# Optimization experiments

Measured on AMD Instinct MI355X. Metric: run time of the kernel, lower is better.

The kernel has to match this reference:

```python
import jax, jax.numpy as jnp
import numpy as np

LATENT = 1024

def setup_inputs() -> dict:
    key = jax.random.key(0)
    ks = jax.random.split(key, 8)
    N, BD, H, W = 1024, 2048, 7, 7
    C = 64  # num classes (pos == orient, required by stack dim=2)
    feat = jax.random.normal(ks[0], (N, BD, H, W), dtype=jnp.float32)
    fc1_w = jax.random.normal(ks[1], (LATENT, BD), dtype=jnp.float32) * (2.0 / BD) ** 0.5
    fc1_b = jnp.zeros((LATENT,), dtype=jnp.float32)
    cls_pos_w = jax.random.normal(ks[2], (C, LATENT), dtype=jnp.float32) * (2.0 / LATENT) ** 0.5
    cls_pos_b = jnp.zeros((C,), dtype=jnp.float32)
    cls_orient_w = jax.random.normal(ks[3], (C, LATENT), dtype=jnp.float32) * (2.0 / LATENT) ** 0.5
    cls_orient_b = jnp.zeros((C,), dtype=jnp.float32)
    reg_pos_w = jax.random.normal(ks[4], (C, 3, LATENT), dtype=jnp.float32) * (2.0 / LATENT) ** 0.5
    reg_pos_b = jnp.zeros((C, 3), dtype=jnp.float32)
    reg_orient_w = jax.random.normal(ks[5], (C, 4, LATENT), dtype=jnp.float32) * (2.0 / LATENT) ** 0.5
    reg_orient_b = jnp.zeros((C, 4), dtype=jnp.float32)
    return {"feat": feat, "fc1_w": fc1_w, "fc1_b": fc1_b,
            "cls_pos_w": cls_pos_w, "cls_pos_b": cls_pos_b,
            "cls_orient_w": cls_orient_w, "cls_orient_b": cls_orient_b,
            "reg_pos_w": reg_pos_w, "reg_pos_b": reg_pos_b,
            "reg_orient_w": reg_orient_w, "reg_orient_b": reg_orient_b}

def _to_label(pred):
    # relu(sum(cumprod(pred > 0.5, dim=1)) - 1) -> int64 ordinal label
    run = jnp.cumprod((pred > 0.5).astype(jnp.int32), axis=1)
    return jnp.maximum(run.sum(axis=1) - 1, 0).astype(jnp.int32)

def reference(feat, fc1_w, fc1_b, cls_pos_w, cls_pos_b, cls_orient_w, cls_orient_b,
              reg_pos_w, reg_pos_b, reg_orient_w, reg_orient_b):
    # AdaptiveAvgPool2d(1) + flatten -> [N, backbone_dim]
    x = feat.mean(axis=(2, 3))
    # fc1 + ReLU (dropout is identity at inference)
    x = jax.nn.relu(x @ fc1_w.T + fc1_b)  # [N, latent]
    cls_x = jax.nn.sigmoid(x @ cls_pos_w.T + cls_pos_b)      # [N, C]
    cls_q = jax.nn.sigmoid(x @ cls_orient_w.T + cls_orient_b)  # [N, C]
    idx_x = _to_label(cls_x)
    idx_q = _to_label(cls_q)
    # Hard-routed expert heads: gather per-sample expert weights, batched matvec
    p_x = jnp.einsum('nkd,nd->nk', reg_pos_w[idx_x], x) + reg_pos_b[idx_x]        # [N, 3]
    p_q = jnp.einsum('nkd,nd->nk', reg_orient_w[idx_q], x) + reg_orient_b[idx_q]  # [N, 4]
    pose = jnp.concatenate([p_x, p_q], axis=1)       # [N, 7]
    pose_cls = jnp.stack([cls_x, cls_q], axis=2)     # [N, C, 2]
    return pose, pose_cls
```

## Files before the change

kernel.cpp:

```cpp
#include <hip/hip_runtime.h>
#include <hip/hip_bf16.h>

#define N_SAMP   1024
#define BD       2048
#define LATENT_D 1024
#define NCLS     64
#define HW       49

typedef __attribute__((ext_vector_type(8))) _Float16 f16x8;
typedef __attribute__((ext_vector_type(4))) float f32x4;
typedef unsigned short u16;

__device__ __forceinline__ size_t split_idx_r(int row, int k, int rows) {
    const int kg = k >> 5, ke = k & 31;
    const int c2 = (ke * 2) ^ (((row >> 1) & 3) << 4);
    return ((size_t)(kg * rows + row) * 32) + (c2 >> 1);
}

__device__ __forceinline__ void split2(float v, u16* p0, u16* p1, size_t idx) {
    _Float16 h0 = (_Float16)v;
    _Float16 h1 = (_Float16)(v - (float)h0);
    p0[idx] = *(u16*)&h0;
    p1[idx] = *(u16*)&h1;
}

#define GLL16(g, l) __builtin_amdgcn_global_load_lds( \
    (const __attribute__((address_space(1))) void*)(g), \
    (__attribute__((address_space(3))) void*)(l), 16, 0, 0)

__global__ __launch_bounds__(256) void prep_kernel(const float* __restrict__ feat,
                                                   const float* __restrict__ W,
                                                   const float* __restrict__ Wp,
                                                   const float* __restrict__ Wo,
                                                   u16* __restrict__ a0,
                                                   u16* __restrict__ a1,
                                                   u16* __restrict__ b0,
                                                   u16* __restrict__ b1,
                                                   u16* __restrict__ c0,
                                                   u16* __restrict__ c1) {
    __shared__ float buf[256 * HW];
    const int b = blockIdx.x;
    const int tid = threadIdx.x;
    if (b < 8192) {
        const int lane = tid & 63, wv = tid >> 6;
        const float* src = feat + (size_t)b * (256 * HW);
        for (int c = wv; c < 49; c += 4)
            GLL16(src + c * 256 + lane * 4, (char*)buf + c * 1024 + lane * 16);
        asm volatile("s_waitcnt vmcnt(0)" ::: "memory");
        __syncthreads();
        const float* p = buf + tid * HW;
        float s = 0.f;
        #pragma unroll
        for (int k = 0; k < HW; ++k) s += p[k];
        const float v = s * (1.0f / 49.0f);
        const int n = b >> 3;
        const int d = (b & 7) * 256 + tid;
        split2(v, a0, a1, split_idx_r(n, d, N_SAMP));
    } else if (b < 16384) {
        const int b2 = b - 8192;
        const int row = b2 >> 3;
        const int d = (b2 & 7) * 256 + tid;
        split2(W[(size_t)row * BD + d], b0, b1, split_idx_r(row, d, LATENT_D));
    } else {
        const int b2 = b - 16384;
        const int row = b2 >> 2;
        const int d = (b2 & 3) * 256 + tid;
        const float v = row < 64 ? Wp[(size_t)row * LATENT_D + d]
                                 : Wo[(size_t)(row - 64) * LATENT_D + d];
        split2(v, c0, c1, split_idx_r(row, d, 128));
    }
}

__global__ __launch_bounds__(256, 2) void split_mfma(
    const u16* __restrict__ A0, const u16* __restrict__ A1,
    const u16* __restrict__ B0, const u16* __restrict__ B1,
    float* __restrict__ part, int ksteps, int rowsA, int rowsB, int ldc) {
    __shared__ u16 lds[2][4 * 4096];
    const int nwg = gridDim.x * gridDim.y * gridDim.z;
    const int flat = blockIdx.x + gridDim.x * (blockIdx.y + gridDim.y * blockIdx.z);
    const int chunk = nwg >> 3;
    const int swz = (flat & 7) * chunk + (flat >> 3);
    const int bn = swz % gridDim.x;
    const int rest = swz / gridDim.x;
    const int bm = rest % gridDim.y;
    const int kz = rest / gridDim.y;

    const int tid = threadIdx.x, lane = tid & 63, wv = tid >> 6;
    const int wrow = (wv >> 1) * 64, wcol = (wv & 1) * 64;
    const int r15 = lane & 15, khi = lane >> 4;

    const u16* gA[2] = {A0, A1};
    const u16* gB[2] = {B0, B1};
    const int kg0 = kz * ksteps;

    auto stage = [&](int kg, int buf) {
        #pragma unroll
        for (int s = 0; s < 2; ++s) {
            const u16* g = gA[s] + ((size_t)(kg * rowsA + bm * 128 + wv * 32) * 32) + lane * 8;
            u16* l = &lds[buf][s * 4096 + wv * 1024 + lane * 8];
            GLL16(g, l);
            GLL16(g + 512, l + 512);
        }
        #pragma unroll
        for (int s = 0; s < 2; ++s) {
            const u16* g = gB[s] + ((size_t)(kg * rowsB + bn * 128 + wv * 32) * 32) + lane * 8;
            u16* l = &lds[buf][(2 + s) * 4096 + wv * 1024 + lane * 8];
            GLL16(g, l);
            GLL16(g + 512, l + 512);
        }
    };

    f32x4 acc[4][4];
    #pragma unroll
    for (int i = 0; i < 4; ++i)
        #pragma unroll
        for (int j = 0; j < 4; ++j) acc[i][j] = (f32x4){0.f, 0.f, 0.f, 0.f};

    stage(kg0, 0);
    asm volatile("s_waitcnt vmcnt(0)" ::: "memory");
    __builtin_amdgcn_s_barrier();

    int cur = 0;
    for (int ks = 0; ks < ksteps; ++ks) {
        f16x8 af[4][2], bf[4][2];
        #pragma unroll
        for (int i = 0; i < 4; ++i) {
            const int rowA = wrow + i * 16 + r15;
            const int offA = rowA * 64 + ((khi * 16) ^ (((rowA >> 1) & 3) << 4));
            const int rowB = wcol + i * 16 + r15;
            const int offB = rowB * 64 + ((khi * 16) ^ (((rowB >> 1) & 3) << 4));
            #pragma unroll
            for (int s = 0; s < 2; ++s) {
                af[i][s] = *(const f16x8*)((const char*)&lds[cur][s * 4096] + offA);
                bf[i][s] = *(const f16x8*)((const char*)&lds[cur][(2 + s) * 4096] + offB);
            }
        }
        if (ks + 1 < ksteps) stage(kg0 + ks + 1, cur ^ 1);
        #pragma unroll
        for (int p = 0; p < 3; ++p) {
            const int pa = (p == 2) ? 1 : 0;
            const int pb = (p == 1) ? 1 : 0;
            #pragma unroll
            for (int i = 0; i < 4; ++i)
                #pragma unroll
                for (int j = 0; j < 4; ++j)
                    acc[i][j] = __builtin_amdgcn_mfma_f32_16x16x32_f16(
                        af[i][pa], bf[j][pb], acc[i][j], 0, 0, 0);
        }
        asm volatile("s_waitcnt vmcnt(0)" ::: "memory");
        __builtin_amdgcn_s_barrier();
        cur ^= 1;
    }

    float* pt = part + (size_t)kz * ((size_t)N_SAMP * ldc);
    #pragma unroll
    for (int i = 0; i < 4; ++i) {
        const int row0 = bm * 128 + wrow + i * 16 + khi * 4;
        #pragma unroll
        for (int j = 0; j < 4; ++j) {
            const int col = bn * 128 + wcol + j * 16 + r15;
            #pragma unroll
            for (int q = 0; q < 4; ++q)
                pt[(size_t)(row0 + q) * ldc + col] = acc[i][j][q];
        }
    }
}

__global__ __launch_bounds__(256) void reduce_fc1(const float* __restrict__ part,
                                                  const float* __restrict__ bias,
                                                  float* __restrict__ x,
                                                  u16* __restrict__ x0,
                                                  u16* __restrict__ x1,
                                                  int nsplit) {
    const int i = blockIdx.x * 256 + threadIdx.x;
    const float4* p = reinterpret_cast<const float4*>(part);
    float4 s = p[i];
    for (int z = 1; z < nsplit; ++z) {
        const float4 t = p[(size_t)z * 262144 + i];
        s.x += t.x; s.y += t.y; s.z += t.z; s.w += t.w;
    }
    const float4 b = reinterpret_cast<const float4*>(bias)[i & 255];
    s.x = fmaxf(s.x + b.x, 0.f); s.y = fmaxf(s.y + b.y, 0.f);
    s.z = fmaxf(s.z + b.z, 0.f); s.w = fmaxf(s.w + b.w, 0.f);
    reinterpret_cast<float4*>(x)[i] = s;
    const int n = i >> 8, d0 = (i & 255) * 4;
    split2(s.x, x0, x1, split_idx_r(n, d0 + 0, N_SAMP));
    split2(s.y, x0, x1, split_idx_r(n, d0 + 1, N_SAMP));
    split2(s.z, x0, x1, split_idx_r(n, d0 + 2, N_SAMP));
    split2(s.w, x0, x1, split_idx_r(n, d0 + 3, N_SAMP));
}

__global__ __launch_bounds__(128) void decode_expert(const float* __restrict__ part2,
                                                     const float* __restrict__ bp,
                                                     const float* __restrict__ bo,
                                                     const float* __restrict__ x,
                                                     const float* __restrict__ wpos,
                                                     const float* __restrict__ bpos,
                                                     const float* __restrict__ wori,
                                                     const float* __restrict__ bori,
                                                     float* __restrict__ pose_cls,
                                                     float* __restrict__ pose,
                                                     int nsplit) {
    const int n = blockIdx.x, t = threadIdx.x;
    __shared__ float xs[LATENT_D];
    __shared__ int esh[2];

    const float4* x4 = reinterpret_cast<const float4*>(x + (size_t)n * LATENT_D);
    float4* xs4 = reinterpret_cast<float4*>(xs);
    xs4[t] = x4[t];
    xs4[t + 128] = x4[t + 128];

    float s = (t < 64) ? bp[t] : bo[t - 64];
    for (int z = 0; z < nsplit; ++z)
        s += part2[(size_t)z * (N_SAMP * 128) + (size_t)n * 128 + t];
    const float sig = 1.0f / (1.0f + expf(-s));
    const int head = t >> 6, c = t & 63;
    pose_cls[(size_t)n * (NCLS * 2) + c * 2 + head] = sig;

    const unsigned long long mask = __ballot(s > 0.0f);
    if (c == 0) {
        const unsigned long long inv = ~mask;
        const int run = inv ? __builtin_ctzll(inv) : 64;
        const int lab = run - 1;
        esh[head] = lab > 0 ? lab : 0;
    }
    __syncthreads();

    const int e = esh[head];
    const int nk = head ? 4 : 3;
    for (int kk = 0; kk < nk; ++kk) {
        const float* wr = head ? wori + (size_t)(e * 4 + kk) * LATENT_D
                               : wpos + (size_t)(e * 3 + kk) * LATENT_D;
        const float bb = head ? bori[e * 4 + kk] : bpos[e * 3 + kk];
        const float4* w4 = reinterpret_cast<const float4*>(wr);
        float s2 = 0.f;
        #pragma unroll
        for (int i = 0; i < 4; ++i) {
            const int q = c + i * 64;
            const float4 a = w4[q];
            s2 += a.x * xs[q * 4] + a.y * xs[q * 4 + 1] + a.z * xs[q * 4 + 2] + a.w * xs[q * 4 + 3];
        }
        #pragma unroll
        for (int off = 32; off > 0; off >>= 1) s2 += __shfl_down(s2, off);
        if (c == 0) pose[(size_t)n * 7 + (head ? 3 + kk : kk)] = s2 + bb;
    }
}

extern "C" void kernel_launch(void* const* d_in, const int* in_sizes, int n_in,
                              void* d_out, int out_size, void* d_ws, size_t ws_size,
                              hipStream_t stream) {
    const float* feat   = (const float*)d_in[0];
    const float* fc1_w  = (const float*)d_in[1];
    const float* fc1_b  = (const float*)d_in[2];
    const float* cpw    = (const float*)d_in[3];
    const float* cpb    = (const float*)d_in[4];
    const float* cow    = (const float*)d_in[5];
    const float* cob    = (const float*)d_in[6];
    const float* rpw    = (const float*)d_in[7];
    const float* rpb    = (const float*)d_in[8];
    const float* row_   = (const float*)d_in[9];
    const float* rob    = (const float*)d_in[10];

    float* out = (float*)d_out;
    float* pose     = out;
    float* pose_cls = out + (size_t)N_SAMP * 7;

    char* ws = (char*)d_ws;
    const size_t MB = (size_t)1 << 20;
    size_t off = 0;
    auto take = [&](size_t bytes) { char* p = ws + off; off += (bytes + 255) & ~(size_t)255; return p; };

    u16* A0 = (u16*)take(4 * MB);
    u16* A1 = (u16*)take(4 * MB);
    u16* B0 = (u16*)take(4 * MB);
    u16* B1 = (u16*)take(4 * MB);
    u16* C0 = (u16*)take(256 * 1024);
    u16* C1 = (u16*)take(256 * 1024);
    u16* X0 = (u16*)take(2 * MB);
    u16* X1 = (u16*)take(2 * MB);
    float* x = (float*)take(4 * MB);

    int nsplit = 8;
    while (nsplit > 1 && off + (size_t)nsplit * 4 * MB + 3 * MB > ws_size) nsplit >>= 1;
    float* part = (float*)take((size_t)nsplit * 4 * MB);
    int nsplit_c = 4;
    while (nsplit_c > 1 && off + (size_t)nsplit_c * 512 * 1024 > ws_size) nsplit_c >>= 1;
    float* part2 = (float*)take((size_t)nsplit_c * 512 * 1024);

    prep_kernel<<<16896, 256, 0, stream>>>(feat, fc1_w, cpw, cow,
                                           A0, A1, B0, B1, C0, C1);
    split_mfma<<<dim3(8, 8, nsplit), 256, 0, stream>>>(
        A0, A1, B0, B1, part, 64 / nsplit, N_SAMP, LATENT_D, LATENT_D);
    reduce_fc1<<<1024, 256, 0, stream>>>(part, fc1_b, x, X0, X1, nsplit);
    split_mfma<<<dim3(1, 8, nsplit_c), 256, 0, stream>>>(
        X0, X1, C0, C1, part2, 32 / nsplit_c, N_SAMP, 128, 128);
    decode_expert<<<N_SAMP, 128, 0, stream>>>(part2, cpb, cob, x, rpw, rpb, row_, rob,
                                              pose_cls, pose, nsplit_c);
}
```

Measured before the change: 133.0 us.

## Add smaller-tile classifier GEMM kernel with deeper split-K and earlier prefetch

Introduces a dedicated 64x64-tile MFMA kernel for the classifier GEMM, launched with many more workgroups and split-K raised to 8, to fill the GPU better than the old 32-workgroup launch. It also moves the next-stage global-to-LDS prefetch ahead of the LDS fragment reads in the main GEMM loop for more overlap. The trade-off is a larger partial-sum buffer and more reduction work in the decode kernel.

```diff
diff --git a/kernel.cpp b/kernel.cpp
--- a/kernel.cpp
+++ b/kernel.cpp
@@ -122,6 +122,7 @@
 
     int cur = 0;
     for (int ks = 0; ks < ksteps; ++ks) {
+        if (ks + 1 < ksteps) stage(kg0 + ks + 1, cur ^ 1);
         f16x8 af[4][2], bf[4][2];
         #pragma unroll
         for (int i = 0; i < 4; ++i) {
@@ -135,7 +136,6 @@
                 bf[i][s] = *(const f16x8*)((const char*)&lds[cur][(2 + s) * 4096] + offB);
             }
         }
-        if (ks + 1 < ksteps) stage(kg0 + ks + 1, cur ^ 1);
         #pragma unroll
         for (int p = 0; p < 3; ++p) {
             const int pa = (p == 2) ? 1 : 0;
@@ -162,6 +162,97 @@
             #pragma unroll
             for (int q = 0; q < 4; ++q)
                 pt[(size_t)(row0 + q) * ldc + col] = acc[i][j][q];
+        }
+    }
+}
+
+__global__ __launch_bounds__(256, 4) void cls_mfma(
+    const u16* __restrict__ A0, const u16* __restrict__ A1,
+    const u16* __restrict__ B0, const u16* __restrict__ B1,
+    float* __restrict__ part, int ksteps) {
+    __shared__ u16 lds[2][4 * 2048];
+    const int nwg = gridDim.x * gridDim.y * gridDim.z;
+    const int flat = blockIdx.x + gridDim.x * (blockIdx.y + gridDim.y * blockIdx.z);
+    const int chunk = nwg >> 3;
+    const int swz = (flat & 7) * chunk + (flat >> 3);
+    const int bn = swz % gridDim.x;
+    const int rest = swz / gridDim.x;
+    const int bm = rest % gridDim.y;
+    const int kz = rest / gridDim.y;
+
+    const int tid = threadIdx.x, lane = tid & 63, wv = tid >> 6;
+    const int wrow = (wv >> 1) * 32, wcol = (wv & 1) * 32;
+    const int r15 = lane & 15, khi = lane >> 4;
+
+    const u16* gA[2] = {A0, A1};
+    const u16* gB[2] = {B0, B1};
+    const int kg0 = kz * ksteps;
+
+    auto stage = [&](int kg, int buf) {
+        #pragma unroll
+        for (int s = 0; s < 2; ++s) {
+            const u16* g = gA[s] + ((size_t)(kg * 1024 + bm * 64 + wv * 16) * 32) + lane * 8;
+            GLL16(g, &lds[buf][s * 2048 + wv * 512 + lane * 8]);
+        }
+        #pragma unroll
+        for (int s = 0; s < 2; ++s) {
+            const u16* g = gB[s] + ((size_t)(kg * 128 + bn * 64 + wv * 16) * 32) + lane * 8;
+            GLL16(g, &lds[buf][(2 + s) * 2048 + wv * 512 + lane * 8]);
+        }
+    };
+
+    f32x4 acc[2][2];
+    #pragma unroll
+    for (int i = 0; i < 2; ++i)
+        #pragma unroll
+        for (int j = 0; j < 2; ++j) acc[i][j] = (f32x4){0.f, 0.f, 0.f, 0.f};
+
+    stage(kg0, 0);
+    asm volatile("s_waitcnt vmcnt(0)" ::: "memory");
+    __builtin_amdgcn_s_barrier();
+
+    int cur = 0;
+    for (int ks = 0; ks < ksteps; ++ks) {
+        if (ks + 1 < ksteps) stage(kg0 + ks + 1, cur ^ 1);
+        f16x8 af[2][2], bf[2][2];
+        #pragma unroll
+        for (int i = 0; i < 2; ++i) {
+            const int rowA = wrow + i * 16 + r15;
+            const int offA = rowA * 64 + ((khi * 16) ^ (((rowA >> 1) & 3) << 4));
+            const int rowB = wcol + i * 16 + r15;
+            const int offB = rowB * 64 + ((khi * 16) ^ (((rowB >> 1) & 3) << 4));
+            #pragma unroll
+            for (int s = 0; s < 2; ++s) {
+                af[i][s] = *(const f16x8*)((const char*)&lds[cur][s * 2048] + offA);
+                bf[i][s] = *(const f16x8*)((const char*)&lds[cur][(2 + s) * 2048] + offB);
+            }
+        }
+        #pragma unroll
+        for (int p = 0; p < 3; ++p) {
+            const int pa = (p == 2) ? 1 : 0;
+            const int pb = (p == 1) ? 1 : 0;
+            #pragma unroll
+            for (int i = 0; i < 2; ++i)
+                #pragma unroll
+                for (int j = 0; j < 2; ++j)
+                    acc[i][j] = __builtin_amdgcn_mfma_f32_16x16x32_f16(
+                        af[i][pa], bf[j][pb], acc[i][j], 0, 0, 0);
+        }
+        asm volatile("s_waitcnt vmcnt(0)" ::: "memory");
+        __builtin_amdgcn_s_barrier();
+        cur ^= 1;
+    }
+
+    float* pt = part + (size_t)kz * ((size_t)N_SAMP * 128);
+    #pragma unroll
+    for (int i = 0; i < 2; ++i) {
+        const int row0 = bm * 64 + wrow + i * 16 + khi * 4;
+        #pragma unroll
+        for (int j = 0; j < 2; ++j) {
+            const int col = bn * 64 + wcol + j * 16 + r15;
+            #pragma unroll
+            for (int q = 0; q < 4; ++q)
+                pt[(size_t)(row0 + q) * 128 + col] = acc[i][j][q];
         }
     }
 }
@@ -281,9 +372,9 @@
     float* x = (float*)take(4 * MB);
 
     int nsplit = 8;
-    while (nsplit > 1 && off + (size_t)nsplit * 4 * MB + 3 * MB > ws_size) nsplit >>= 1;
+    while (nsplit > 1 && off + (size_t)nsplit * 4 * MB + 5 * MB > ws_size) nsplit >>= 1;
     float* part = (float*)take((size_t)nsplit * 4 * MB);
-    int nsplit_c = 4;
+    int nsplit_c = 8;
     while (nsplit_c > 1 && off + (size_t)nsplit_c * 512 * 1024 > ws_size) nsplit_c >>= 1;
     float* part2 = (float*)take((size_t)nsplit_c * 512 * 1024);
 
@@ -292,8 +383,8 @@
     split_mfma<<<dim3(8, 8, nsplit), 256, 0, stream>>>(
         A0, A1, B0, B1, part, 64 / nsplit, N_SAMP, LATENT_D, LATENT_D);
     reduce_fc1<<<1024, 256, 0, stream>>>(part, fc1_b, x, X0, X1, nsplit);
-    split_mfma<<<dim3(1, 8, nsplit_c), 256, 0, stream>>>(
-        X0, X1, C0, C1, part2, 32 / nsplit_c, N_SAMP, 128, 128);
+    cls_mfma<<<dim3(2, 16, nsplit_c), 256, 0, stream>>>(
+        X0, X1, C0, C1, part2, 32 / nsplit_c);
     decode_expert<<<N_SAMP, 128, 0, stream>>>(part2, cpb, cob, x, rpw, rpb, row_, rob,
                                               pose_cls, pose, nsplit_c);
 }
```

New measurement: 128.6 us. -3.3%, faster.

## Fuse fc1 reduction, classifier GEMM and expert decode into one tail kernel

Applied to the files above, without the earlier changes.

Replaces the reduce_fc1, second split-K MFMA GEMM and decode_expert launches with a single tail kernel that, per block of 4 samples, reduces the fc1 split-K partials, applies bias+ReLU, splits to fp16 pairs in LDS, runs the classifier MFMA with double-buffered weight staging, then does the sigmoid/label and expert matvecs. The main GEMM loop is also restructured to issue the next stage's loads before waiting with a partial vmcnt, overlapping loads with compute, and the fc1 split-K factor drops from 8 to 4. This removes intermediate global round trips and launches, at the cost of using only 16 of 64 MFMA rows in the tail and less parallelism in the fc1 GEMM.

```diff
diff --git a/kernel.cpp b/kernel.cpp
--- a/kernel.cpp
+++ b/kernel.cpp
@@ -117,11 +117,17 @@
         for (int j = 0; j < 4; ++j) acc[i][j] = (f32x4){0.f, 0.f, 0.f, 0.f};
 
     stage(kg0, 0);
-    asm volatile("s_waitcnt vmcnt(0)" ::: "memory");
-    __builtin_amdgcn_s_barrier();
 
     int cur = 0;
     for (int ks = 0; ks < ksteps; ++ks) {
+        if (ks + 1 < ksteps) {
+            stage(kg0 + ks + 1, cur ^ 1);
+            asm volatile("s_waitcnt vmcnt(8)" ::: "memory");
+        } else {
+            asm volatile("s_waitcnt vmcnt(0)" ::: "memory");
+        }
+        __builtin_amdgcn_s_barrier();
+        __builtin_amdgcn_sched_barrier(0);
         f16x8 af[4][2], bf[4][2];
         #pragma unroll
         for (int i = 0; i < 4; ++i) {
@@ -135,7 +141,6 @@
                 bf[i][s] = *(const f16x8*)((const char*)&lds[cur][(2 + s) * 4096] + offB);
             }
         }
-        if (ks + 1 < ksteps) stage(kg0 + ks + 1, cur ^ 1);
         #pragma unroll
         for (int p = 0; p < 3; ++p) {
             const int pa = (p == 2) ? 1 : 0;
@@ -147,7 +152,6 @@
                     acc[i][j] = __builtin_amdgcn_mfma_f32_16x16x32_f16(
                         af[i][pa], bf[j][pb], acc[i][j], 0, 0, 0);
         }
-        asm volatile("s_waitcnt vmcnt(0)" ::: "memory");
         __builtin_amdgcn_s_barrier();
         cur ^= 1;
     }
@@ -166,83 +170,144 @@
     }
 }
 
-__global__ __launch_bounds__(256) void reduce_fc1(const float* __restrict__ part,
-                                                  const float* __restrict__ bias,
-                                                  float* __restrict__ x,
-                                                  u16* __restrict__ x0,
-                                                  u16* __restrict__ x1,
-                                                  int nsplit) {
-    const int i = blockIdx.x * 256 + threadIdx.x;
-    const float4* p = reinterpret_cast<const float4*>(part);
-    float4 s = p[i];
-    for (int z = 1; z < nsplit; ++z) {
-        const float4 t = p[(size_t)z * 262144 + i];
-        s.x += t.x; s.y += t.y; s.z += t.z; s.w += t.w;
-    }
-    const float4 b = reinterpret_cast<const float4*>(bias)[i & 255];
-    s.x = fmaxf(s.x + b.x, 0.f); s.y = fmaxf(s.y + b.y, 0.f);
-    s.z = fmaxf(s.z + b.z, 0.f); s.w = fmaxf(s.w + b.w, 0.f);
-    reinterpret_cast<float4*>(x)[i] = s;
-    const int n = i >> 8, d0 = (i & 255) * 4;
-    split2(s.x, x0, x1, split_idx_r(n, d0 + 0, N_SAMP));
-    split2(s.y, x0, x1, split_idx_r(n, d0 + 1, N_SAMP));
-    split2(s.z, x0, x1, split_idx_r(n, d0 + 2, N_SAMP));
-    split2(s.w, x0, x1, split_idx_r(n, d0 + 3, N_SAMP));
-}
-
-__global__ __launch_bounds__(128) void decode_expert(const float* __restrict__ part2,
-                                                     const float* __restrict__ bp,
-                                                     const float* __restrict__ bo,
-                                                     const float* __restrict__ x,
-                                                     const float* __restrict__ wpos,
-                                                     const float* __restrict__ bpos,
-                                                     const float* __restrict__ wori,
-                                                     const float* __restrict__ bori,
-                                                     float* __restrict__ pose_cls,
-                                                     float* __restrict__ pose,
-                                                     int nsplit) {
-    const int n = blockIdx.x, t = threadIdx.x;
-    __shared__ float xs[LATENT_D];
-    __shared__ int esh[2];
-
-    const float4* x4 = reinterpret_cast<const float4*>(x + (size_t)n * LATENT_D);
-    float4* xs4 = reinterpret_cast<float4*>(xs);
-    xs4[t] = x4[t];
-    xs4[t + 128] = x4[t + 128];
-
-    float s = (t < 64) ? bp[t] : bo[t - 64];
-    for (int z = 0; z < nsplit; ++z)
-        s += part2[(size_t)z * (N_SAMP * 128) + (size_t)n * 128 + t];
-    const float sig = 1.0f / (1.0f + expf(-s));
-    const int head = t >> 6, c = t & 63;
-    pose_cls[(size_t)n * (NCLS * 2) + c * 2 + head] = sig;
-
-    const unsigned long long mask = __ballot(s > 0.0f);
-    if (c == 0) {
-        const unsigned long long inv = ~mask;
-        const int run = inv ? __builtin_ctzll(inv) : 64;
-        const int lab = run - 1;
-        esh[head] = lab > 0 ? lab : 0;
+__global__ __launch_bounds__(256) void tail_kernel(
+    const float* __restrict__ part, int nsplit,
+    const float* __restrict__ fc1_b,
+    const u16* __restrict__ C0, const u16* __restrict__ C1,
+    const float* __restrict__ cpb, const float* __restrict__ cob,
+    const float* __restrict__ wpos, const float* __restrict__ bpos,
+    const float* __restrict__ wori, const float* __restrict__ bori,
+    float* __restrict__ pose, float* __restrict__ pose_cls) {
+    __shared__ u16 xs0[4][1024];
+    __shared__ u16 xs1[4][1024];
+    __shared__ float xf[4][1024];
+    __shared__ u16 cl[2][2][4096];
+    __shared__ float lg[4][128];
+    __shared__ int esh[4][2];
+
+    const int b = blockIdx.x;
+    const int tid = threadIdx.x, lane = tid & 63, wv = tid >> 6;
+    const int r15 = lane & 15, khi = lane >> 4;
+    const int row0 = b * 4;
+
+    auto stageC = [&](int kg, int buf) {
+        const u16* g0 = C0 + (size_t)kg * 4096 + tid * 8;
+        GLL16(g0, &cl[buf][0][tid * 8]);
+        GLL16(g0 + 2048, &cl[buf][0][tid * 8 + 2048]);
+        const u16* g1 = C1 + (size_t)kg * 4096 + tid * 8;
+        GLL16(g1, &cl[buf][1][tid * 8]);
+        GLL16(g1 + 2048, &cl[buf][1][tid * 8 + 2048]);
+    };
+
+    stageC(0, 0);
+
+    #pragma unroll
+    for (int i = 0; i < 4; ++i) {
+        const int f = tid + 256 * i;
+        const int r = f >> 8, c4 = f & 255;
+        const float* pp = part + (size_t)(row0 + r) * LATENT_D + c4 * 4;
+        float4 s = *(const float4*)pp;
+        for (int z = 1; z < nsplit; ++z) {
+            const float4 t2 = *(const float4*)(pp + (size_t)z * (N_SAMP * LATENT_D));
+            s.x += t2.x; s.y += t2.y; s.z += t2.z; s.w += t2.w;
+        }
+        const float4 bb = reinterpret_cast<const float4*>(fc1_b)[c4];
+        s.x = fmaxf(s.x + bb.x, 0.f); s.y = fmaxf(s.y + bb.y, 0.f);
+        s.z = fmaxf(s.z + bb.z, 0.f); s.w = fmaxf(s.w + bb.w, 0.f);
+        *reinterpret_cast<float4*>(&xf[r][c4 * 4]) = s;
+        const int k0 = c4 * 4;
+        split2(s.x, &xs0[0][0], &xs1[0][0], r * 1024 + k0 + 0);
+        split2(s.y, &xs0[0][0], &xs1[0][0], r * 1024 + k0 + 1);
+        split2(s.z, &xs0[0][0], &xs1[0][0], r * 1024 + k0 + 2);
+        split2(s.w, &xs0[0][0], &xs1[0][0], r * 1024 + k0 + 3);
     }
     __syncthreads();
 
-    const int e = esh[head];
-    const int nk = head ? 4 : 3;
-    for (int kk = 0; kk < nk; ++kk) {
-        const float* wr = head ? wori + (size_t)(e * 4 + kk) * LATENT_D
-                               : wpos + (size_t)(e * 3 + kk) * LATENT_D;
-        const float bb = head ? bori[e * 4 + kk] : bpos[e * 3 + kk];
+    f32x4 acc[2];
+    acc[0] = (f32x4){0.f, 0.f, 0.f, 0.f};
+    acc[1] = (f32x4){0.f, 0.f, 0.f, 0.f};
+    const int rA = r15 & 3;
+
+    int cur = 0;
+    for (int ks = 0; ks < 32; ++ks) {
+        if (ks + 1 < 32) {
+            stageC(ks + 1, cur ^ 1);
+            asm volatile("s_waitcnt vmcnt(4)" ::: "memory");
+        } else {
+            asm volatile("s_waitcnt vmcnt(0)" ::: "memory");
+        }
+        __builtin_amdgcn_s_barrier();
+        __builtin_amdgcn_sched_barrier(0);
+        const int aoff = rA * 2048 + ks * 64 + khi * 16;
+        const f16x8 a0 = *(const f16x8*)((const char*)xs0 + aoff);
+        const f16x8 a1 = *(const f16x8*)((const char*)xs1 + aoff);
+        #pragma unroll
+        for (int j = 0; j < 2; ++j) {
+            const int col = wv * 32 + j * 16 + r15;
+            const int offB = col * 64 + ((khi * 16) ^ (((col >> 1) & 3) << 4));
+            const f16x8 b0 = *(const f16x8*)((const char*)&cl[cur][0][0] + offB);
+            const f16x8 b1 = *(const f16x8*)((const char*)&cl[cur][1][0] + offB);
+            acc[j] = __builtin_amdgcn_mfma_f32_16x16x32_f16(a0, b0, acc[j], 0, 0, 0);
+            acc[j] = __builtin_amdgcn_mfma_f32_16x16x32_f16(a0, b1, acc[j], 0, 0, 0);
+            acc[j] = __builtin_amdgcn_mfma_f32_16x16x32_f16(a1, b0, acc[j], 0, 0, 0);
+        }
+        __builtin_amdgcn_s_barrier();
+        cur ^= 1;
+    }
+
+    if (lane < 16) {
+        #pragma unroll
+        for (int j = 0; j < 2; ++j)
+            #pragma unroll
+            for (int q = 0; q < 4; ++q)
+                lg[q][wv * 32 + j * 16 + lane] = acc[j][q];
+    }
+    __syncthreads();
+
+    if (tid < 128) {
+        const int head = tid >> 6, c = tid & 63;
+        #pragma unroll
+        for (int q = 0; q < 4; ++q) {
+            const float s = lg[q][tid] + (head ? cob[c] : cpb[c]);
+            const float sig = 1.0f / (1.0f + expf(-s));
+            pose_cls[(size_t)(row0 + q) * (NCLS * 2) + c * 2 + head] = sig;
+            const unsigned long long mask = __ballot(s > 0.0f);
+            if (c == 0) {
+                const unsigned long long inv = ~mask;
+                const int run = inv ? __builtin_ctzll(inv) : 64;
+                const int lab = run - 1;
+                esh[q][head] = lab > 0 ? lab : 0;
+            }
+        }
+    }
+    __syncthreads();
+
+    for (int task = wv; task < 28; task += 4) {
+        const int q = task / 7, k = task % 7;
+        const float* wr;
+        float bb;
+        if (k < 3) {
+            const int e = esh[q][0];
+            wr = wpos + (size_t)(e * 3 + k) * LATENT_D;
+            bb = bpos[e * 3 + k];
+        } else {
+            const int e = esh[q][1];
+            const int kk = k - 3;
+            wr = wori + (size_t)(e * 4 + kk) * LATENT_D;
+            bb = bori[e * 4 + kk];
+        }
         const float4* w4 = reinterpret_cast<const float4*>(wr);
         float s2 = 0.f;
         #pragma unroll
         for (int i = 0; i < 4; ++i) {
-            const int q = c + i * 64;
-            const float4 a = w4[q];
-            s2 += a.x * xs[q * 4] + a.y * xs[q * 4 + 1] + a.z * xs[q * 4 + 2] + a.w * xs[q * 4 + 3];
+            const int qq = lane + i * 64;
+            const float4 a = w4[qq];
+            s2 += a.x * xf[q][qq * 4] + a.y * xf[q][qq * 4 + 1]
+                + a.z * xf[q][qq * 4 + 2] + a.w * xf[q][qq * 4 + 3];
         }
         #pragma unroll
         for (int off = 32; off > 0; off >>= 1) s2 += __shfl_down(s2, off);
-        if (c == 0) pose[(size_t)n * 7 + (head ? 3 + kk : kk)] = s2 + bb;
+        if (lane == 0) pose[(size_t)(row0 + q) * 7 + k] = s2 + bb;
     }
 }
 
@@ -276,24 +341,16 @@
     u16* B1 = (u16*)take(4 * MB);
     u16* C0 = (u16*)take(256 * 1024);
     u16* C1 = (u16*)take(256 * 1024);
-    u16* X0 = (u16*)take(2 * MB);
-    u16* X1 = (u16*)take(2 * MB);
-    float* x = (float*)take(4 * MB);
-
-    int nsplit = 8;
-    while (nsplit > 1 && off + (size_t)nsplit * 4 * MB + 3 * MB > ws_size) nsplit >>= 1;
+
+    int nsplit = 4;
+    while (nsplit > 1 && off + (size_t)nsplit * 4 * MB > ws_size) nsplit >>= 1;
     float* part = (float*)take((size_t)nsplit * 4 * MB);
-    int nsplit_c = 4;
-    while (nsplit_c > 1 && off + (size_t)nsplit_c * 512 * 1024 > ws_size) nsplit_c >>= 1;
-    float* part2 = (float*)take((size_t)nsplit_c * 512 * 1024);
 
     prep_kernel<<<16896, 256, 0, stream>>>(feat, fc1_w, cpw, cow,
                                            A0, A1, B0, B1, C0, C1);
     split_mfma<<<dim3(8, 8, nsplit), 256, 0, stream>>>(
         A0, A1, B0, B1, part, 64 / nsplit, N_SAMP, LATENT_D, LATENT_D);
-    reduce_fc1<<<1024, 256, 0, stream>>>(part, fc1_b, x, X0, X1, nsplit);
-    split_mfma<<<dim3(1, 8, nsplit_c), 256, 0, stream>>>(
-        X0, X1, C0, C1, part2, 32 / nsplit_c, N_SAMP, 128, 128);
-    decode_expert<<<N_SAMP, 128, 0, stream>>>(part2, cpb, cob, x, rpw, rpb, row_, rob,
-                                              pose_cls, pose, nsplit_c);
-}
+    tail_kernel<<<256, 256, 0, stream>>>(part, nsplit, fc1_b, C0, C1,
+                                         cpb, cob, rpw, rpb, row_, rob,
+                                         pose, pose_cls);
+}
```

Result: no change. 130.4 us (-1.9%).
